# Optimization experiments

Hardware: AMD Instinct MI355X
Metric: run time of the kernel (lower is better)

The kernel has to match this reference:

```python
import jax, jax.numpy as jnp
import numpy as np

T, B = 80, 256                 # timesteps (max objs per image), num sequences (images)
OBJ_DIM, EMBED, HID = 4096, 200, 512
NCLS = 151                      # 150 VG classes + background
D = HID + OBJ_DIM + EMBED + 128 # decoder inputs_dim = 4936


def _packed_gather_idx():
    # descending lengths 80..41, mimicking a sorted PackedSequence
    lengths = np.array([T - (i * 40) // B for i in range(B)])
    idx = []
    for t in range(T):
        bs = int((lengths > t).sum())
        idx.extend(t * B + b for b in range(bs))
    return np.asarray(idx, dtype=np.int32)  # [15504]


def setup_inputs() -> dict:
    key = jax.random.key(0)
    ks = jax.random.split(key, 6)
    s = jnp.float32(0.02)
    return {
        "sequence": jax.random.normal(ks[0], (T, B, D), jnp.float32),
        "embed": jax.random.normal(ks[1], (NCLS + 1, EMBED), jnp.float32) * s,
        "W_in": jax.random.normal(ks[2], (6 * HID, D + EMBED), jnp.float32) * s,
        "b_in": jnp.zeros((6 * HID,), jnp.float32),
        "W_state": jax.random.normal(ks[3], (5 * HID, HID), jnp.float32) * s,
        "b_state": jnp.zeros((5 * HID,), jnp.float32),
        "W_out": jax.random.normal(ks[4], (NCLS, HID), jnp.float32) * s,
        "b_out": jnp.zeros((NCLS,), jnp.float32),
        "gather_idx": jnp.asarray(_packed_gather_idx()),
    }


def reference(sequence, embed, W_in, b_in, W_state, b_state, W_out, b_out, gather_idx):
    H = HID

    def step(carry, x_t):
        h, c, prev_embed = carry
        ti = jnp.concatenate([x_t, prev_embed], axis=1)          # [B, D+E]
        pi = ti @ W_in.T + b_in                                   # [B, 6H]
        ps = h @ W_state.T + b_state                              # [B, 5H]
        i_g = jax.nn.sigmoid(pi[:, 0*H:1*H] + ps[:, 0*H:1*H])
        f_g = jax.nn.sigmoid(pi[:, 1*H:2*H] + ps[:, 1*H:2*H])
        m_i = jnp.tanh(pi[:, 2*H:3*H] + ps[:, 2*H:3*H])
        o_g = jax.nn.sigmoid(pi[:, 3*H:4*H] + ps[:, 3*H:4*H])
        c_new = i_g * m_i + f_g * c
        out = o_g * jnp.tanh(c_new)
        hw_g = jax.nn.sigmoid(pi[:, 4*H:5*H] + ps[:, 4*H:5*H])
        h_new = hw_g * out + (1.0 - hw_g) * pi[:, 5*H:6*H]        # highway
        pred = h_new @ W_out.T + b_out                            # [B, NCLS]
        # softmax is monotonic: argmax of softmax(pred)[:,1:] == argmax of pred[:,1:]
        best = jnp.argmax(pred[:, 1:], axis=1) + 1                # [B], in [1, NCLS-1]
        pe_new = embed[best + 1]                                  # [B, E]
        return (h_new, c_new, pe_new), (pred, best)

    h0 = jnp.zeros((B, HID), sequence.dtype)
    c0 = jnp.zeros((B, HID), sequence.dtype)
    pe0 = jnp.broadcast_to(embed[0], (B, EMBED))                  # 'start' token embed
    _, (dists, commits) = jax.lax.scan(step, (h0, c0, pe0), sequence)
    # packed (timestep-major) flattening of valid entries only
    out_dists = dists.reshape(T * B, NCLS)[gather_idx]            # [N, NCLS]
    out_commits = commits.reshape(T * B)[gather_idx]              # [N]
    return out_dists, out_commits
```

## Files before the change

kernel.cpp:

```cpp
#include <hip/hip_runtime.h>
#include <cstddef>
#include <cstdint>

#define T_STEPS 80
#define BATCH   256
#define DIM     4936
#define EMB     200
#define DE      5136
#define HID     512
#define SIXH    3072
#define FIVEH   2560
#define NCLS    151
#define NPACK   15504
#define NKT     156
#define NKT_H   16
#define NCOMB   2816
#define BUFSZ   24576

typedef unsigned short ushort_t;
typedef short short8 __attribute__((ext_vector_type(8)));
typedef float f32x4 __attribute__((ext_vector_type(4)));

__device__ inline ushort_t f2bf_rn(float x) {
    union { float f; uint32_t u; } v; v.f = x;
    uint32_t u = v.u;
    return (ushort_t)((u + 0x7FFFu + ((u >> 16) & 1u)) >> 16);
}
__device__ inline float bf2f(ushort_t b) {
    union { float f; uint32_t u; } v; v.u = ((uint32_t)b) << 16;
    return v.f;
}
__device__ inline float sigmoidf(float x) { return 1.f / (1.f + expf(-x)); }

__global__ __launch_bounds__(256) void convert_split(
    const float* __restrict__ src, int ld, int kvalid,
    ushort_t* __restrict__ hi, ushort_t* __restrict__ lo, int nktiles)
{
    __shared__ float s[128][33];
    const int tid = threadIdx.x;
    const int kt  = blockIdx.x;
    const int mt  = blockIdx.y;

#pragma unroll
    for (int it = 0; it < 4; ++it) {
        int idx = it * 256 + tid;
        int row = idx >> 3;
        int f4  = idx & 7;
        int k   = kt * 32 + f4 * 4;
        const float* p = src + (size_t)(mt * 128 + row) * ld + k;
        float4 v;
        if (k + 3 < kvalid) v = *(const float4*)p;
        else {
            v.x = (k + 0) < kvalid ? p[0] : 0.f;
            v.y = (k + 1) < kvalid ? p[1] : 0.f;
            v.z = (k + 2) < kvalid ? p[2] : 0.f;
            v.w = (k + 3) < kvalid ? p[3] : 0.f;
        }
        s[row][f4 * 4 + 0] = v.x; s[row][f4 * 4 + 1] = v.y;
        s[row][f4 * 4 + 2] = v.z; s[row][f4 * 4 + 3] = v.w;
    }
    __syncthreads();

    const size_t base = ((size_t)mt * nktiles + kt) * 4096;
#pragma unroll
    for (int it = 0; it < 2; ++it) {
        int o   = it * 256 + tid;
        int kb  = o >> 7;
        int row = o & 127;
        alignas(16) ushort_t hbuf[8];
        alignas(16) ushort_t lbuf[8];
#pragma unroll
        for (int e = 0; e < 8; ++e) {
            float x = s[row][kb * 8 + e];
            ushort_t hh = f2bf_rn(x);
            float lof = x - bf2f(hh);
            hbuf[e] = hh;
            lbuf[e] = f2bf_rn(lof);
        }
        *(uint4*)(hi + base + (size_t)o * 8) = *(const uint4*)hbuf;
        *(uint4*)(lo + base + (size_t)o * 8) = *(const uint4*)lbuf;
    }
}

__device__ inline void gload16(const ushort_t* g, ushort_t* l) {
    __builtin_amdgcn_global_load_lds(
        (const __attribute__((address_space(1))) void*)g,
        (__attribute__((address_space(3))) void*)l, 16, 0, 0);
}

__global__ __launch_bounds__(512, 1) void mfma3(
    const ushort_t* __restrict__ Ah, const ushort_t* __restrict__ Al,
    const ushort_t* __restrict__ Bh, const ushort_t* __restrict__ Bl,
    const float* __restrict__ bias, float* __restrict__ OUT,
    int nkt, int ldout)
{
    extern __shared__ __align__(16) ushort_t smem[];

    const int tid  = threadIdx.x;
    const int wave = tid >> 6;
    const int lane = tid & 63;
    const int ntb = blockIdx.x, mtb = blockIdx.y;
    const int wr = wave >> 1, wc = wave & 1;

    f32x4 acc[4][4];
#pragma unroll
    for (int i = 0; i < 4; ++i)
#pragma unroll
        for (int j = 0; j < 4; ++j) acc[i][j] = (f32x4){0.f, 0.f, 0.f, 0.f};

    const size_t a0 = (size_t)(2 * mtb) * nkt * 4096;
    const size_t a1 = a0 + (size_t)nkt * 4096;
    const size_t bb = (size_t)ntb * nkt * 4096;

    const int kb = lane >> 4;
    const int lr = lane & 15;
    const int aoffl = (wr >> 1) * 4096 + kb * 1024 + ((wr & 1) * 64 + lr) * 8;
    const int boffl = kb * 1024 + (wc * 64 + lr) * 8;

#define STAGE3(slot, kt_) do {                                      \
        ushort_t* d = smem + (slot) * BUFSZ;                        \
        const size_t ko = (size_t)(kt_) * 4096 + tid * 8;           \
        gload16(Ah + a0 + ko, d + tid * 8);                         \
        gload16(Ah + a1 + ko, d + 4096 + tid * 8);                  \
        gload16(Al + a0 + ko, d + 8192 + tid * 8);                  \
        gload16(Al + a1 + ko, d + 12288 + tid * 8);                 \
        gload16(Bh + bb + ko, d + 16384 + tid * 8);                 \
        gload16(Bl + bb + ko, d + 20480 + tid * 8);                 \
    } while (0)

    STAGE3(0, 0);
    if (nkt > 1) STAGE3(1, 1);

    int cb = 0;
    for (int kt = 0; kt < nkt; ++kt) {
        if (kt < nkt - 1) asm volatile("s_waitcnt vmcnt(6)" ::: "memory");
        else              asm volatile("s_waitcnt vmcnt(0)" ::: "memory");
        __builtin_amdgcn_sched_barrier(0);
        __builtin_amdgcn_s_barrier();
        if (kt + 2 < nkt) {
            int s2 = cb + 2; if (s2 >= 3) s2 -= 3;
            STAGE3(s2, kt + 2);
        }

        const ushort_t* p  = smem + cb * BUFSZ;
        const ushort_t* pB = p + 16384;
        short8 ah[4], al[4], bh[4], bl[4];
#pragma unroll
        for (int i = 0; i < 4; ++i) {
            ah[i] = *(const short8*)&p[aoffl + i * 128];
            al[i] = *(const short8*)&p[8192 + aoffl + i * 128];
        }
#pragma unroll
        for (int j = 0; j < 4; ++j) {
            bh[j] = *(const short8*)&pB[boffl + j * 128];
            bl[j] = *(const short8*)&pB[4096 + boffl + j * 128];
        }
#pragma unroll
        for (int i = 0; i < 4; ++i)
#pragma unroll
            for (int j = 0; j < 4; ++j) {
                acc[i][j] = __builtin_amdgcn_mfma_f32_16x16x32_bf16(ah[i], bh[j], acc[i][j], 0, 0, 0);
                acc[i][j] = __builtin_amdgcn_mfma_f32_16x16x32_bf16(ah[i], bl[j], acc[i][j], 0, 0, 0);
                acc[i][j] = __builtin_amdgcn_mfma_f32_16x16x32_bf16(al[i], bh[j], acc[i][j], 0, 0, 0);
            }

        cb = (cb == 2) ? 0 : cb + 1;
    }
#undef STAGE3

#pragma unroll
    for (int i = 0; i < 4; ++i) {
        const int row = mtb * 256 + wr * 64 + i * 16 + (lane >> 4) * 4;
#pragma unroll
        for (int j = 0; j < 4; ++j) {
            const int col = ntb * 128 + wc * 64 + j * 16 + (lane & 15);
            const float bv = bias[col];
#pragma unroll
            for (int r = 0; r < 4; ++r)
                OUT[(size_t)(row + r) * ldout + col] = acc[i][j][r] + bv;
        }
    }
}

__global__ __launch_bounds__(256) void ps_splitk(
    const ushort_t* __restrict__ hH, const ushort_t* __restrict__ hL,
    const ushort_t* __restrict__ WcH, const ushort_t* __restrict__ WcL,
    float* __restrict__ partial)
{
    __shared__ ushort_t sAh[8192], sAl[8192], sBh[8192], sBl[8192];

    const int tid  = threadIdx.x;
    const int wave = tid >> 6;
    const int lane = tid & 63;
    const int ntile = blockIdx.x;
    const int mtile = blockIdx.y;
    const int ks    = blockIdx.z;
    const int amt = mtile >> 1, arh = mtile & 1;
    const int bmt = ntile >> 1, brh = ntile & 1;
    const int wr = wave >> 1, wc = wave & 1;

    f32x4 acc[2][2];
#pragma unroll
    for (int i = 0; i < 2; ++i)
#pragma unroll
        for (int j = 0; j < 2; ++j) acc[i][j] = (f32x4){0.f, 0.f, 0.f, 0.f};

    const int lw    = wave * 512;
    const int lsrcA = wave * 1024 + arh * 512 + lane * 8;
    const int lsrcB = wave * 1024 + brh * 512 + lane * 8;

#pragma unroll
    for (int ki = 0; ki < 4; ++ki) {
        const int kt = ks * 4 + ki;
        const size_t atile = ((size_t)(amt * NKT_H + kt)) * 4096;
        const size_t btile = ((size_t)(bmt * NKT_H + kt)) * 4096;
        gload16(hH  + atile + lsrcA, &sAh[ki * 2048 + lw]);
        gload16(hL  + atile + lsrcA, &sAl[ki * 2048 + lw]);
        gload16(WcH + btile + lsrcB, &sBh[ki * 2048 + lw]);
        gload16(WcL + btile + lsrcB, &sBl[ki * 2048 + lw]);
    }
    __syncthreads();

    const int kb = lane >> 4;
    const int lr = lane & 15;
#pragma unroll
    for (int ki = 0; ki < 4; ++ki) {
        short8 ah[2], al[2], bh[2], bl[2];
#pragma unroll
        for (int i = 0; i < 2; ++i) {
            const int ao = ki * 2048 + kb * 512 + (wr * 32 + i * 16 + lr) * 8;
            ah[i] = *(const short8*)&sAh[ao];
            al[i] = *(const short8*)&sAl[ao];
        }
#pragma unroll
        for (int j = 0; j < 2; ++j) {
            const int bo = ki * 2048 + kb * 512 + (wc * 32 + j * 16 + lr) * 8;
            bh[j] = *(const short8*)&sBh[bo];
            bl[j] = *(const short8*)&sBl[bo];
        }
#pragma unroll
        for (int i = 0; i < 2; ++i)
#pragma unroll
            for (int j = 0; j < 2; ++j) {
                acc[i][j] = __builtin_amdgcn_mfma_f32_16x16x32_bf16(ah[i], bh[j], acc[i][j], 0, 0, 0);
                acc[i][j] = __builtin_amdgcn_mfma_f32_16x16x32_bf16(ah[i], bl[j], acc[i][j], 0, 0, 0);
                acc[i][j] = __builtin_amdgcn_mfma_f32_16x16x32_bf16(al[i], bh[j], acc[i][j], 0, 0, 0);
            }
    }

    float* out = partial + ((size_t)ks * 256 + mtile * 64) * NCOMB + ntile * 64;
#pragma unroll
    for (int i = 0; i < 2; ++i) {
        const int row = wr * 32 + i * 16 + (lane >> 4) * 4;
#pragma unroll
        for (int j = 0; j < 2; ++j) {
            const int col = wc * 32 + j * 16 + (lane & 15);
#pragma unroll
            for (int r = 0; r < 4; ++r)
                out[(size_t)(row + r) * NCOMB + col] = acc[i][j][r];
        }
    }
}

__global__ __launch_bounds__(256) void ew_gemm(
    const float* __restrict__ embed, const float* __restrict__ Win,
    float* __restrict__ EW)
{
    __shared__ float As[16][68];
    __shared__ float Bs[16][68];
    const int tid = threadIdx.x;
    const int tx  = tid & 15;
    const int ty  = tid >> 4;
    const int n0  = blockIdx.x * 64;
    const int m0  = blockIdx.y * 64;
    const int lrow = tid >> 2;
    const int lk   = (tid & 3) * 4;

    float acc[4][4];
#pragma unroll
    for (int i = 0; i < 4; ++i)
#pragma unroll
        for (int j = 0; j < 4; ++j) acc[i][j] = 0.f;

    for (int k0 = 0; k0 < EMB; k0 += 16) {
        int k = k0 + lk;
        float4 av = {0.f,0.f,0.f,0.f}, bv = {0.f,0.f,0.f,0.f};
        if (k < EMB) {
            int am = m0 + lrow;
            if (am < 152) av = *(const float4*)(embed + (size_t)am * EMB + k);
            bv = *(const float4*)(Win + (size_t)(n0 + lrow) * DE + DIM + k);
        }
        __syncthreads();
        As[lk + 0][lrow] = av.x; As[lk + 1][lrow] = av.y;
        As[lk + 2][lrow] = av.z; As[lk + 3][lrow] = av.w;
        Bs[lk + 0][lrow] = bv.x; Bs[lk + 1][lrow] = bv.y;
        Bs[lk + 2][lrow] = bv.z; Bs[lk + 3][lrow] = bv.w;
        __syncthreads();
#pragma unroll
        for (int kk = 0; kk < 16; ++kk) {
            float4 a4 = *(const float4*)&As[kk][ty * 4];
            float4 b4 = *(const float4*)&Bs[kk][tx * 4];
            float avr[4] = {a4.x, a4.y, a4.z, a4.w};
            float bvr[4] = {b4.x, b4.y, b4.z, b4.w};
#pragma unroll
            for (int i = 0; i < 4; ++i)
#pragma unroll
                for (int j = 0; j < 4; ++j)
                    acc[i][j] = fmaf(avr[i], bvr[j], acc[i][j]);
        }
    }
#pragma unroll
    for (int i = 0; i < 4; ++i) {
        int m = m0 + ty * 4 + i;
        if (m < 152) {
#pragma unroll
            for (int j = 0; j < 4; ++j)
                EW[(size_t)m * SIXH + n0 + tx * 4 + j] = acc[i][j];
        }
    }
}

__global__ __launch_bounds__(256) void pad_wout(
    const float* __restrict__ Wout, float* __restrict__ padW)
{
    int i = blockIdx.x * 256 + threadIdx.x;
    if (i < 256 * 512) {
        int row = i >> 9;
        padW[i] = (row < NCLS) ? Wout[i] : 0.f;
    }
}

__global__ __launch_bounds__(256) void init_state(
    float* __restrict__ c, ushort_t* __restrict__ hHt, ushort_t* __restrict__ hLt)
{
    int i = blockIdx.x * 256 + threadIdx.x;
    if (i < BATCH * HID) { c[i] = 0.f; hHt[i] = 0; hLt[i] = 0; }
}

__global__ __launch_bounds__(256) void step_fused(
    const float* __restrict__ px_t,
    const float* __restrict__ EW,
    const float* __restrict__ partial,
    const float* __restrict__ b_state,
    const float* __restrict__ b_out,
    int first,
    ushort_t* __restrict__ hHt, ushort_t* __restrict__ hLt,
    float* __restrict__ c, float* __restrict__ hF,
    float* __restrict__ dists_prev,
    int*   __restrict__ commit_prev)
{
    __shared__ float hs[HID];
    __shared__ float preds_s[NCLS + 1];
    __shared__ int   commit_sh;

    const int tid = threadIdx.x;
    const int b   = blockIdx.x;

    int erow = 0;
    if (!first) {
        if (tid < NCLS) {
            const float* pq = partial + (size_t)b * NCOMB + 2560;
            float pr = b_out[tid] + pq[tid]
                     + pq[(size_t)256 * NCOMB + tid]
                     + pq[(size_t)2 * 256 * NCOMB + tid]
                     + pq[(size_t)3 * 256 * NCOMB + tid];
            preds_s[tid] = pr;
            dists_prev[(size_t)b * NCLS + tid] = pr;
        }
        __syncthreads();
        if (tid == 0) {
            int bi = 1; float bv = preds_s[1];
            for (int n = 2; n < NCLS; ++n) {
                float v = preds_s[n];
                if (v > bv) { bv = v; bi = n; }
            }
            commit_prev[b] = bi;
            commit_sh = bi;
        }
        __syncthreads();
        erow = commit_sh + 1;
    }

    const float* ew = EW + (size_t)erow * SIXH;
    const float* px = px_t + (size_t)b * SIXH;
    const float* pp = partial + (size_t)b * NCOMB;

#pragma unroll
    for (int it = 0; it < 2; ++it) {
        const int u = it * 256 + tid;
        float p[6];
#pragma unroll
        for (int k2 = 0; k2 < 5; ++k2) {
            const int o = k2 * HID + u;
            float s = pp[o] + pp[(size_t)256 * NCOMB + o]
                    + pp[(size_t)2 * 256 * NCOMB + o] + pp[(size_t)3 * 256 * NCOMB + o];
            p[k2] = px[o] + ew[o] + s + b_state[o];
        }
        p[5] = px[5 * HID + u] + ew[5 * HID + u];

        float i_g = sigmoidf(p[0]);
        float f_g = sigmoidf(p[1]);
        float m_i = tanhf(p[2]);
        float o_g = sigmoidf(p[3]);
        float c_new = i_g * m_i + f_g * c[(size_t)b * HID + u];
        float outv  = o_g * tanhf(c_new);
        float hw    = sigmoidf(p[4]);
        float h_new = hw * outv + (1.f - hw) * p[5];
        c[(size_t)b * HID + u]  = c_new;
        hF[(size_t)b * HID + u] = h_new;
        hs[u] = h_new;
    }
    __syncthreads();

    if (tid < 128) {
        const int half = tid >> 6;
        const int ch   = tid & 63;
        const int mt   = b >> 7;
        const int row  = b & 127;
        const size_t off = ((size_t)(mt * NKT_H + (ch >> 2))) * 4096
                         + (size_t)(ch & 3) * 1024 + (size_t)row * 8;
        alignas(16) ushort_t buf[8];
        if (half == 0) {
#pragma unroll
            for (int e = 0; e < 8; ++e) buf[e] = f2bf_rn(hs[ch * 8 + e]);
            *(uint4*)(hHt + off) = *(const uint4*)buf;
        } else {
#pragma unroll
            for (int e = 0; e < 8; ++e) {
                float x = hs[ch * 8 + e];
                buf[e] = f2bf_rn(x - bf2f(f2bf_rn(x)));
            }
            *(uint4*)(hLt + off) = *(const uint4*)buf;
        }
    }
}

__global__ __launch_bounds__(192) void finalize_last(
    const float* __restrict__ hF, const float* __restrict__ Wout,
    const float* __restrict__ b_out,
    float* __restrict__ dists_last, int* __restrict__ commits_last)
{
    __shared__ float hsh[HID];
    __shared__ float preds[NCLS + 1];
    const int b = blockIdx.x;
    const int tid = threadIdx.x;

    if (tid < 128) {
        float4 v = *(const float4*)(hF + (size_t)b * HID + tid * 4);
        *(float4*)&hsh[tid * 4] = v;
    }
    __syncthreads();
    if (tid < NCLS) {
        const float* w = Wout + (size_t)tid * HID;
        float s0 = 0.f, s1 = 0.f, s2 = 0.f, s3 = 0.f;
        for (int k = 0; k < HID; k += 4) {
            float4 w4 = *(const float4*)(w + k);
            float4 h4 = *(const float4*)&hsh[k];
            s0 = fmaf(h4.x, w4.x, s0);
            s1 = fmaf(h4.y, w4.y, s1);
            s2 = fmaf(h4.z, w4.z, s2);
            s3 = fmaf(h4.w, w4.w, s3);
        }
        float s = b_out[tid] + ((s0 + s1) + (s2 + s3));
        preds[tid] = s;
        dists_last[(size_t)b * NCLS + tid] = s;
    }
    __syncthreads();
    if (tid == 0) {
        int bi = 1; float bv = preds[1];
        for (int n = 2; n < NCLS; ++n) {
            float v = preds[n];
            if (v > bv) { bv = v; bi = n; }
        }
        commits_last[b] = bi;
    }
}

__global__ __launch_bounds__(192) void gather_out(
    const float* __restrict__ dists, const int* __restrict__ commits,
    const int* __restrict__ gidx, float* __restrict__ out)
{
    const int i = blockIdx.x;
    const int g = gidx[i];
    if (threadIdx.x < NCLS)
        out[(size_t)i * NCLS + threadIdx.x] = dists[(size_t)g * NCLS + threadIdx.x];
    if (threadIdx.x == NCLS)
        out[(size_t)NPACK * NCLS + i] = (float)commits[g];
}

extern "C" void kernel_launch(void* const* d_in, const int* in_sizes, int n_in,
                              void* d_out, int out_size, void* d_ws, size_t ws_size,
                              hipStream_t stream)
{
    const float* X      = (const float*)d_in[0];
    const float* embed  = (const float*)d_in[1];
    const float* Win    = (const float*)d_in[2];
    const float* b_in   = (const float*)d_in[3];
    const float* Wst    = (const float*)d_in[4];
    const float* b_st   = (const float*)d_in[5];
    const float* Wout   = (const float*)d_in[6];
    const float* b_out  = (const float*)d_in[7];
    const int*   gidx   = (const int*)d_in[8];

    hipFuncSetAttribute((const void*)mfma3,
                        hipFuncAttributeMaxDynamicSharedMemorySize,
                        3 * BUFSZ * 2);

    const size_t WN  = (size_t)24 * NKT * 4096;
    const size_t WCN = (size_t)22 * NKT_H * 4096;
    const size_t HN  = (size_t)2 * NKT_H * 4096;

    ushort_t* Wh  = (ushort_t*)d_ws;
    ushort_t* Wl  = Wh + WN;
    ushort_t* WcH = Wl + WN;
    ushort_t* WcL = WcH + WCN;
    ushort_t* hHt = WcL + WCN;
    ushort_t* hLt = hHt + HN;
    float* EW      = (float*)(hLt + HN);
    float* partial = EW + (size_t)152 * SIXH;
    float* c       = partial + (size_t)4 * BATCH * NCOMB;
    float* hF      = c + (size_t)BATCH * HID;
    float* padW    = hF + (size_t)BATCH * HID;
    float* dists   = padW + (size_t)256 * HID;
    int* commits   = (int*)(dists + (size_t)T_STEPS * BATCH * NCLS);
    char* cbase    = (char*)(commits + T_STEPS * BATCH);

    size_t off = (size_t)(cbase - (char*)d_ws);
    off = (off + 255) & ~(size_t)255;
    const size_t per_t = (size_t)2 * 2 * NKT * 4096 * 2 + (size_t)BATCH * SIXH * 4;
    size_t rem = (ws_size > off) ? (ws_size - off) : 0;
    int CT = (int)(rem / per_t);
    if (CT > T_STEPS) CT = T_STEPS;
    if (CT < 1) CT = 1;

    ushort_t* Xh = (ushort_t*)((char*)d_ws + off);
    ushort_t* Xl = Xh + (size_t)2 * CT * NKT * 4096;
    float* px    = (float*)(Xl + (size_t)2 * CT * NKT * 4096);

    convert_split<<<dim3(NKT, 24), 256, 0, stream>>>(Win, DE, DIM, Wh, Wl, NKT);
    convert_split<<<dim3(NKT_H, 20), 256, 0, stream>>>(Wst, HID, HID, WcH, WcL, NKT_H);
    pad_wout<<<512, 256, 0, stream>>>(Wout, padW);
    convert_split<<<dim3(NKT_H, 2), 256, 0, stream>>>(
        padW, HID, HID, WcH + (size_t)20 * NKT_H * 4096, WcL + (size_t)20 * NKT_H * 4096, NKT_H);
    ew_gemm<<<dim3(SIXH / 64, 3), 256, 0, stream>>>(embed, Win, EW);
    init_state<<<512, 256, 0, stream>>>(c, hHt, hLt);

    for (int t0 = 0; t0 < T_STEPS; t0 += CT) {
        int nt = T_STEPS - t0;
        if (nt > CT) nt = CT;
        convert_split<<<dim3(NKT, 2 * nt), 256, 0, stream>>>(
            X + (size_t)t0 * BATCH * DIM, DIM, DIM, Xh, Xl, NKT);
        mfma3<<<dim3(SIXH / 128, nt), 512, 3 * BUFSZ * 2, stream>>>(
            Xh, Xl, Wh, Wl, b_in, px, NKT, SIXH);
        for (int t = t0; t < t0 + nt; ++t) {
            const int tp = (t > 0) ? t - 1 : 0;
            ps_splitk<<<dim3(44, 4, 4), 256, 0, stream>>>(
                hHt, hLt, WcH, WcL, partial);
            step_fused<<<BATCH, 256, 0, stream>>>(
                px + (size_t)(t - t0) * BATCH * SIXH, EW, partial, b_st, b_out,
                (t == 0) ? 1 : 0, hHt, hLt, c, hF,
                dists + (size_t)tp * BATCH * NCLS, commits + (size_t)tp * BATCH);
        }
    }

    finalize_last<<<BATCH, 192, 0, stream>>>(
        hF, Wout, b_out,
        dists + (size_t)(T_STEPS - 1) * BATCH * NCLS,
        commits + (size_t)(T_STEPS - 1) * BATCH);

    gather_out<<<NPACK, 192, 0, stream>>>(dists, commits, gidx, (float*)d_out);
}
```

Baseline: 3.259 ms.

## Enlarge input-projection GEMM tile to 256x256 with 32x32 MFMA and double buffering

The split-bf16 input-projection GEMM now computes a 256x256 output tile per block instead of 256x128, with each wave owning a 128x64 subtile built from 32x32x16 MFMAs. The three-slot LDS ring with a two-ahead prefetch is replaced by two 64KB buffers and a one-ahead prefetch that waits on vmcnt(0) every iteration. The larger tile raises operand reuse and halves the B-side re-reads, but it also halves the grid to 12 x nt blocks and leaves less load/compute overlap.

After: 3.211 ms. No clear change (-1.5%).

```diff
diff --git a/kernel.cpp b/kernel.cpp
--- a/kernel.cpp
+++ b/kernel.cpp
@@ -15,11 +15,12 @@
 #define NKT     156
 #define NKT_H   16
 #define NCOMB   2816
-#define BUFSZ   24576
+#define BUF2SZ  32768
 
 typedef unsigned short ushort_t;
 typedef short short8 __attribute__((ext_vector_type(8)));
 typedef float f32x4 __attribute__((ext_vector_type(4)));
+typedef float f32x16 __attribute__((ext_vector_type(16)));
 
 __device__ inline ushort_t f2bf_rn(float x) {
     union { float f; uint32_t u; } v; v.f = x;
@@ -100,86 +101,91 @@
     const int wave = tid >> 6;
     const int lane = tid & 63;
     const int ntb = blockIdx.x, mtb = blockIdx.y;
-    const int wr = wave >> 1, wc = wave & 1;
-
-    f32x4 acc[4][4];
+    const int wr = wave >> 2;
+    const int wc = wave & 3;
+
+    f32x16 acc[4][2];
 #pragma unroll
     for (int i = 0; i < 4; ++i)
 #pragma unroll
-        for (int j = 0; j < 4; ++j) acc[i][j] = (f32x4){0.f, 0.f, 0.f, 0.f};
+        for (int j = 0; j < 2; ++j)
+#pragma unroll
+            for (int r = 0; r < 16; ++r) acc[i][j][r] = 0.f;
 
     const size_t a0 = (size_t)(2 * mtb) * nkt * 4096;
     const size_t a1 = a0 + (size_t)nkt * 4096;
-    const size_t bb = (size_t)ntb * nkt * 4096;
-
-    const int kb = lane >> 4;
-    const int lr = lane & 15;
-    const int aoffl = (wr >> 1) * 4096 + kb * 1024 + ((wr & 1) * 64 + lr) * 8;
-    const int boffl = kb * 1024 + (wc * 64 + lr) * 8;
-
-#define STAGE3(slot, kt_) do {                                      \
-        ushort_t* d = smem + (slot) * BUFSZ;                        \
+    const size_t b0 = (size_t)(2 * ntb) * nkt * 4096;
+    const size_t b1 = b0 + (size_t)nkt * 4096;
+
+#define STAGE2(slot, kt_) do {                                      \
+        ushort_t* d = smem + (slot) * BUF2SZ;                       \
         const size_t ko = (size_t)(kt_) * 4096 + tid * 8;           \
         gload16(Ah + a0 + ko, d + tid * 8);                         \
         gload16(Ah + a1 + ko, d + 4096 + tid * 8);                  \
         gload16(Al + a0 + ko, d + 8192 + tid * 8);                  \
         gload16(Al + a1 + ko, d + 12288 + tid * 8);                 \
-        gload16(Bh + bb + ko, d + 16384 + tid * 8);                 \
-        gload16(Bl + bb + ko, d + 20480 + tid * 8);                 \
+        gload16(Bh + b0 + ko, d + 16384 + tid * 8);                 \
+        gload16(Bh + b1 + ko, d + 20480 + tid * 8);                 \
+        gload16(Bl + b0 + ko, d + 24576 + tid * 8);                 \
+        gload16(Bl + b1 + ko, d + 28672 + tid * 8);                 \
     } while (0)
 
-    STAGE3(0, 0);
-    if (nkt > 1) STAGE3(1, 1);
-
-    int cb = 0;
+    const int lrow = lane & 31;
+    const int kg   = lane >> 5;
+    const int aBase = wr * 4096;
+    const int bBase = 16384 + (wc >> 1) * 4096;
+    const int bCol  = (wc & 1) * 64;
+
+    STAGE2(0, 0);
+
     for (int kt = 0; kt < nkt; ++kt) {
-        if (kt < nkt - 1) asm volatile("s_waitcnt vmcnt(6)" ::: "memory");
-        else              asm volatile("s_waitcnt vmcnt(0)" ::: "memory");
+        asm volatile("s_waitcnt vmcnt(0)" ::: "memory");
         __builtin_amdgcn_sched_barrier(0);
         __builtin_amdgcn_s_barrier();
-        if (kt + 2 < nkt) {
-            int s2 = cb + 2; if (s2 >= 3) s2 -= 3;
-            STAGE3(s2, kt + 2);
-        }
-
-        const ushort_t* p  = smem + cb * BUFSZ;
-        const ushort_t* pB = p + 16384;
-        short8 ah[4], al[4], bh[4], bl[4];
-#pragma unroll
-        for (int i = 0; i < 4; ++i) {
-            ah[i] = *(const short8*)&p[aoffl + i * 128];
-            al[i] = *(const short8*)&p[8192 + aoffl + i * 128];
-        }
-#pragma unroll
-        for (int j = 0; j < 4; ++j) {
-            bh[j] = *(const short8*)&pB[boffl + j * 128];
-            bl[j] = *(const short8*)&pB[4096 + boffl + j * 128];
-        }
-#pragma unroll
-        for (int i = 0; i < 4; ++i)
-#pragma unroll
-            for (int j = 0; j < 4; ++j) {
-                acc[i][j] = __builtin_amdgcn_mfma_f32_16x16x32_bf16(ah[i], bh[j], acc[i][j], 0, 0, 0);
-                acc[i][j] = __builtin_amdgcn_mfma_f32_16x16x32_bf16(ah[i], bl[j], acc[i][j], 0, 0, 0);
-                acc[i][j] = __builtin_amdgcn_mfma_f32_16x16x32_bf16(al[i], bh[j], acc[i][j], 0, 0, 0);
+        if (kt + 1 < nkt) STAGE2((kt + 1) & 1, kt + 1);
+
+        const ushort_t* p = smem + (kt & 1) * BUF2SZ;
+#pragma unroll
+        for (int kh = 0; kh < 2; ++kh) {
+            const int ko = (kh * 2 + kg) * 1024;
+            short8 a_h[4], a_l[4], b_h[2], b_l[2];
+#pragma unroll
+            for (int ms = 0; ms < 4; ++ms) {
+                const int ao = aBase + ko + (ms * 32 + lrow) * 8;
+                a_h[ms] = *(const short8*)&p[ao];
+                a_l[ms] = *(const short8*)&p[8192 + ao];
             }
-
-        cb = (cb == 2) ? 0 : cb + 1;
-    }
-#undef STAGE3
-
-#pragma unroll
-    for (int i = 0; i < 4; ++i) {
-        const int row = mtb * 256 + wr * 64 + i * 16 + (lane >> 4) * 4;
-#pragma unroll
-        for (int j = 0; j < 4; ++j) {
-            const int col = ntb * 128 + wc * 64 + j * 16 + (lane & 15);
+#pragma unroll
+            for (int ns = 0; ns < 2; ++ns) {
+                const int bo = bBase + ko + (bCol + ns * 32 + lrow) * 8;
+                b_h[ns] = *(const short8*)&p[bo];
+                b_l[ns] = *(const short8*)&p[8192 + bo];
+            }
+#pragma unroll
+            for (int ms = 0; ms < 4; ++ms)
+#pragma unroll
+                for (int ns = 0; ns < 2; ++ns) {
+                    acc[ms][ns] = __builtin_amdgcn_mfma_f32_32x32x16_bf16(a_h[ms], b_h[ns], acc[ms][ns], 0, 0, 0);
+                    acc[ms][ns] = __builtin_amdgcn_mfma_f32_32x32x16_bf16(a_h[ms], b_l[ns], acc[ms][ns], 0, 0, 0);
+                    acc[ms][ns] = __builtin_amdgcn_mfma_f32_32x32x16_bf16(a_l[ms], b_h[ns], acc[ms][ns], 0, 0, 0);
+                }
+        }
+    }
+#undef STAGE2
+
+#pragma unroll
+    for (int ms = 0; ms < 4; ++ms)
+#pragma unroll
+        for (int ns = 0; ns < 2; ++ns) {
+            const int col = ntb * 256 + wc * 64 + ns * 32 + (lane & 31);
             const float bv = bias[col];
-#pragma unroll
-            for (int r = 0; r < 4; ++r)
-                OUT[(size_t)(row + r) * ldout + col] = acc[i][j][r] + bv;
-        }
-    }
+            const int rowb = mtb * 256 + wr * 128 + ms * 32 + 4 * (lane >> 5);
+#pragma unroll
+            for (int r = 0; r < 16; ++r) {
+                const int row = rowb + (r & 3) + 8 * (r >> 2);
+                OUT[(size_t)row * ldout + col] = acc[ms][ns][r] + bv;
+            }
+        }
 }
 
 __global__ __launch_bounds__(256) void ps_splitk(
@@ -504,7 +510,7 @@
 
     hipFuncSetAttribute((const void*)mfma3,
                         hipFuncAttributeMaxDynamicSharedMemorySize,
-                        3 * BUFSZ * 2);
+                        2 * BUF2SZ * 2);
 
     const size_t WN  = (size_t)24 * NKT * 4096;
     const size_t WCN = (size_t)22 * NKT_H * 4096;
@@ -550,7 +556,7 @@
         if (nt > CT) nt = CT;
         convert_split<<<dim3(NKT, 2 * nt), 256, 0, stream>>>(
             X + (size_t)t0 * BATCH * DIM, DIM, DIM, Xh, Xl, NKT);
-        mfma3<<<dim3(SIXH / 128, nt), 512, 3 * BUFSZ * 2, stream>>>(
+        mfma3<<<dim3(SIXH / 256, nt), 512, 2 * BUF2SZ * 2, stream>>>(
             Xh, Xl, Wh, Wl, b_in, px, NKT, SIXH);
         for (int t = t0; t < t0 + nt; ++t) {
             const int tp = (t > 0) ? t - 1 : 0;
```
